# Kernel optimization log

Measured on AMD Instinct MI355X. Metric: run time of the kernel, lower is better.

Reference implementation:

```python
import jax, jax.numpy as jnp
import numpy as np

LSTM = 256
NUM_CELLS = 5
BLOCKS = 6
TEMP = 5.0
TANH_C = 1.1


def setup_inputs() -> dict:
    key = jax.random.key(0)
    ks = jax.random.split(key, 8)
    s = 0.05  # small init so sigmoids/tanh stay in sane range
    return {
        "enc_w": jax.random.normal(ks[0], (5, LSTM), jnp.float32) * s,
        "w_ih": jax.random.normal(ks[1], (4 * LSTM, LSTM), jnp.float32) * s,
        "w_hh": jax.random.normal(ks[2], (4 * LSTM, LSTM), jnp.float32) * s,
        "b_ih": jax.random.normal(ks[3], (4 * LSTM,), jnp.float32) * s,
        "b_hh": jax.random.normal(ks[4], (4 * LSTM,), jnp.float32) * s,
        "w1": jax.random.normal(ks[5], (LSTM, LSTM), jnp.float32) * s,
        "w2": jax.random.normal(ks[6], (LSTM, LSTM), jnp.float32) * s,
        "v": jax.random.normal(ks[7], (LSTM,), jnp.float32) * s,
    }


def _lstm_cell(x, h, c, w_ih, w_hh, b_ih, b_hh):
    # torch.nn.LSTMCell gate order: i, f, g, o
    g = w_ih @ x + b_ih + w_hh @ h + b_hh  # [4*LSTM]
    i, f, gg, o = jnp.split(g, 4)
    i, f, o = jax.nn.sigmoid(i), jax.nn.sigmoid(f), jax.nn.sigmoid(o)
    c2 = f * c + i * jnp.tanh(gg)
    h2 = o * jnp.tanh(c2)
    return h2, c2


def _run_sampler(bkey, enc_w, w_ih, w_hh, b_ih, b_hh, w1, w2, v):
    zeros = jnp.zeros((LSTM,), jnp.float32)
    inputs = enc_w[0]  # encoder(0)
    anchors = []
    anchors_w1 = []
    prev_h = prev_c = zeros
    # first two layers: LSTM always fed zero state (faithful to source)
    for _ in range(2):
        prev_h, prev_c = _lstm_cell(inputs, zeros, zeros, w_ih, w_hh, b_ih, b_hh)
        anchors.append(zeros)
        anchors_w1.append(w1 @ prev_h)
    arc_seq, log_probs, entropies = [], [], []
    step = 0
    for layer_id in range(2, NUM_CELLS + 2):
        for _ in range(2):
            prev_h, prev_c = _lstm_cell(inputs, prev_h, prev_c, w_ih, w_hh, b_ih, b_hh)
            q = jnp.tanh(jnp.stack(anchors_w1[:layer_id]) + w2 @ prev_h)  # [layer_id, LSTM]
            logits = (q @ v) / TEMP  # [layer_id]
            logits = TANH_C * jnp.tanh(logits)
            skey = jax.random.fold_in(bkey, step); step += 1
            index = jax.random.categorical(skey, logits)
            lsm = jax.nn.log_softmax(logits)
            arc_seq.append(index)
            log_probs.append(-lsm[index])  # F.cross_entropy
            entropies.append(jax.lax.stop_gradient(-jnp.sum(lsm * jnp.exp(lsm))))
            inputs = jnp.stack(anchors[:layer_id])[index]
        prev_h, prev_c = _lstm_cell(inputs, prev_h, prev_c, w_ih, w_hh, b_ih, b_hh)
        anchors.append(prev_h)
        anchors_w1.append(w1 @ prev_h)
        inputs = enc_w[0]
    arc = jnp.stack(arc_seq)  # [2*NUM_CELLS] int
    return arc, sum(entropies), sum(log_probs), prev_c, prev_h


def reference(enc_w, w_ih, w_hh, b_ih, b_hh, w1, w2, v):
    key = jax.random.key(42)
    all_arc = []
    all_entropy = jnp.float32(0.0)
    all_log_prob = jnp.float32(0.0)
    c = h = None
    for b in range(BLOCKS):
        arc, ent, lp, c, h = _run_sampler(
            jax.random.fold_in(key, b), enc_w, w_ih, w_hh, b_ih, b_hh, w1, w2, v)
        all_arc.append(arc)
        all_entropy = all_entropy + ent
        all_log_prob = all_log_prob + lp
    return (jnp.stack(all_arc), all_log_prob, all_entropy, c[None, :], h[None, :])
```

## Files before the change

kernel.cpp:

```cpp
#include <hip/hip_runtime.h>
#include <stdint.h>


#define NBLK  6
#define PWG   8
#define TINYF 1.17549435e-38f
#define FXS   67108864.0f
#define READY_MAGIC 0x52454459
#define DONE_MAGIC  0x444f4e45

#define OFF_READY 0u
#define OFF_DONE  192u
#define OFF_PART  224u
#define OFF_HP    320u
#define OFF_ACC   24896u

typedef unsigned long long u64;
struct U2 { uint32_t x, y; };

__device__ __forceinline__ U2 tf2x32(uint32_t k0, uint32_t k1,
                                     uint32_t c0, uint32_t c1) {
  uint32_t ks2 = k0 ^ k1 ^ 0x1BD11BDAu;
  uint32_t x0 = c0 + k0, x1 = c1 + k1;
#define TFR(r) { x0 += x1; x1 = (x1 << (r)) | (x1 >> (32 - (r))); x1 ^= x0; }
  TFR(13) TFR(15) TFR(26) TFR(6)   x0 += k1;  x1 += ks2 + 1u;
  TFR(17) TFR(29) TFR(16) TFR(24)  x0 += ks2; x1 += k0 + 2u;
  TFR(13) TFR(15) TFR(26) TFR(6)   x0 += k0;  x1 += k1 + 3u;
  TFR(17) TFR(29) TFR(16) TFR(24)  x0 += k1;  x1 += ks2 + 4u;
  TFR(13) TFR(15) TFR(26) TFR(6)   x0 += ks2; x1 += k0 + 5u;
#undef TFR
  U2 r; r.x = x0; r.y = x1; return r;
}

__device__ __forceinline__ float sigf(float x) {
  return 1.0f / (1.0f + expf(-x));
}
__device__ __forceinline__ void istore(int* p, int v) {
  __hip_atomic_store(p, v, __ATOMIC_RELAXED, __HIP_MEMORY_SCOPE_AGENT);
}
__device__ __forceinline__ int iload(const int* p) {
  return __hip_atomic_load(p, __ATOMIC_RELAXED, __HIP_MEMORY_SCOPE_AGENT);
}
__device__ __forceinline__ void hstore(u64* p, u64 v) {
  __hip_atomic_store(p, v, __ATOMIC_RELAXED, __HIP_MEMORY_SCOPE_AGENT);
}
__device__ __forceinline__ u64 hload(const u64* p) {
  return __hip_atomic_load(p, __ATOMIC_RELAXED, __HIP_MEMORY_SCOPE_AGENT);
}
__device__ __forceinline__ void fstore(float* p, float v) {
  __hip_atomic_store(p, v, __ATOMIC_RELAXED, __HIP_MEMORY_SCOPE_AGENT);
}
__device__ __forceinline__ float fload(const float* p) {
  return __hip_atomic_load(p, __ATOMIC_RELAXED, __HIP_MEMORY_SCOPE_AGENT);
}

__global__ __launch_bounds__(1024) void ctrl_fused(
    const float* __restrict__ enc_w,
    const float* __restrict__ wih,
    const float* __restrict__ whh,
    const float* __restrict__ b_ih,
    const float* __restrict__ b_hh,
    const float* __restrict__ w1,
    const float* __restrict__ w2,
    const float* __restrict__ vvec,
    unsigned char* __restrict__ ws,
    float* __restrict__ out) {

  const int b = blockIdx.x & 7;
  const int p = blockIdx.x >> 3;
  if (b >= NBLK) return;
  const int tid = threadIdx.x;

  int*   ready = (int*)(ws + OFF_READY);
  int*   done  = (int*)(ws + OFF_DONE);
  float* part  = (float*)(ws + OFF_PART);
  u64*   hp    = (u64*)(ws + OFF_HP);
  int*   acc   = (int*)(ws + OFF_ACC);

  const int rl = tid >> 3, s = tid & 7;
  const int g = rl >> 5, el = rl & 31;
  const int row = g * 256 + p * 32 + el;
  const int k0 = s * 32;
  const int rr = tid & 255, ks = tid >> 2 >> 6;

  __shared__ __align__(16) float hL[256], encL[256], vL[256];
  __shared__ __align__(16) float anchL[4][256];
  __shared__ __align__(16) float partL[1024];
  __shared__ __align__(16) float w2hS[256], aw1S[6][256];
  __shared__ float rowSumL[128], biasS[128], h2S[32];
  __shared__ float logitL[8];
  __shared__ int   selL;

  if (tid < 256) { encL[tid] = enc_w[tid]; vL[tid] = vvec[tid]; }
  if (tid < 128) {
    int gg = tid >> 5, ee = tid & 31, r = gg * 256 + p * 32 + ee;
    biasS[tid] = b_ih[r] + b_hh[r];
  }

  float4 wihr[8], whhr[8];
  #pragma unroll
  for (int c = 0; c < 8; ++c) {
    int cc = (c + s) & 7;
    wihr[c] = *(const float4*)(wih + row * 256 + k0 + cc * 4);
    whhr[c] = *(const float4*)(whh + row * 256 + k0 + cc * 4);
  }
  float w1c[8], w2c[8];
  #pragma unroll
  for (int j = 0; j < 8; ++j) {
    w1c[j] = w1[rr * 256 + p * 32 + ks * 8 + j];
    w2c[j] = w2[rr * 256 + p * 32 + ks * 8 + j];
  }

  if (tid < 32) istore(&acc[1 * (NBLK * 256) + b * 256 + p * 32 + tid], 0);
  __syncthreads();
  if (tid == 0) istore(&ready[b * 8 + p], READY_MAGIC);
  if (tid < 8) {
    while (iload(&ready[b * 8 + tid]) != READY_MAGIC)
      __builtin_amdgcn_s_sleep(1);
  }
  __syncthreads();

  auto dotIH = [&](const float* x) {
    float a = 0.0f;
    #pragma unroll
    for (int c = 0; c < 8; ++c) {
      int cc = (c + s) & 7;
      float4 xv = *(const float4*)(x + k0 + cc * 4);
      float4 w = wihr[c];
      a += w.x * xv.x + w.y * xv.y + w.z * xv.z + w.w * xv.w;
    }
    return a;
  };
  auto dotHH = [&]() {
    float a = 0.0f;
    #pragma unroll
    for (int c = 0; c < 8; ++c) {
      int cc = (c + s) & 7;
      float4 xv = *(const float4*)(hL + k0 + cc * 4);
      float4 w = whhr[c];
      a += w.x * xv.x + w.y * xv.y + w.z * xv.z + w.w * xv.w;
    }
    return a;
  };

  const float encih = dotIH(encL);

  float cv = 0.0f;
  U2 bk = tf2x32(0u, 42u, 0u, (uint32_t)b);
  int k = 1, step = 0;
  float lpAcc = 0.0f, entAcc = 0.0f;

  auto cell = [&](float gacc, int mode, int aid, int cid) {
    partL[tid] = gacc;
    __syncthreads();
    if (tid < 128) {
      float ssum = 0.0f;
      #pragma unroll
      for (int j = 0; j < 8; ++j) ssum += partL[tid * 8 + j];
      rowSumL[tid] = ssum + biasS[tid];
    }
    __syncthreads();
    if (tid < 32) {
      float gi = rowSumL[tid],       gf = rowSumL[32 + tid];
      float gg2 = rowSumL[64 + tid], go = rowSumL[96 + tid];
      float c2 = sigf(gf) * cv + sigf(gi) * tanhf(gg2);
      float h2 = sigf(go) * tanhf(c2);
      cv = c2;
      h2S[tid] = h2;
      if (mode == 2 && b == NBLK - 1) {
        out[62 + p * 32 + tid] = cv;
        out[318 + p * 32 + tid] = h2;
      }
    }
    __syncthreads();
    if (mode == 2) return;

    {
      const float* wc = (mode == 1) ? w1c : w2c;
      float yp = 0.0f;
      #pragma unroll
      for (int j = 0; j < 8; ++j) yp += wc[j] * h2S[ks * 8 + j];
      atomicAdd(&acc[(k % 3) * (NBLK * 256) + b * 256 + rr],
                __float2int_rn(yp * FXS));
      if (tid < 32)
        istore(&acc[((k + 1) % 3) * (NBLK * 256) + b * 256 + p * 32 + tid], 0);
    }
    __syncthreads();
    if (tid < 32) {
      u64 pk = ((u64)(uint32_t)k << 32) | (u64)__float_as_uint(h2S[tid]);
      hstore(&hp[(k & 1) * (NBLK * 256) + b * 256 + p * 32 + tid], pk);
    }
    if (tid < 256) {
      u64 v;
      const u64* src = &hp[(k & 1) * (NBLK * 256) + b * 256 + tid];
      while ((int)(hload(src) >> 32) != k) __builtin_amdgcn_s_sleep(1);
      v = hload(src);
      float hv = __uint_as_float((uint32_t)v);
      hL[tid] = hv;
      if (mode == 1 && cid >= 0) anchL[cid][tid] = hv;
    }
    __syncthreads();
    if (tid < 256) {
      int iv = iload(&acc[(k % 3) * (NBLK * 256) + b * 256 + tid]);
      float f = (float)((double)iv * (1.0 / 67108864.0));
      if (mode == 1) aw1S[aid][tid] = f; else w2hS[tid] = f;
    }
    __syncthreads();
    ++k;
  };

  auto sample = [&](int L) -> int {
    int wv = tid >> 6, lane = tid & 63;
    if (wv < L) {
      float a = 0.0f;
      #pragma unroll
      for (int j = 0; j < 4; ++j) {
        int kk = lane * 4 + j;
        a += tanhf(aw1S[wv][kk] + w2hS[kk]) * vL[kk];
      }
      a += __shfl_down(a, 32);
      a += __shfl_down(a, 16);
      a += __shfl_down(a, 8);
      a += __shfl_down(a, 4);
      a += __shfl_down(a, 2);
      a += __shfl_down(a, 1);
      if (lane == 0) logitL[wv] = a;
    }
    __syncthreads();
    if (tid < 64) {
      float lg = 0.0f, sgum = -1e30f;
      if (tid < L) {
        lg = 1.1f * tanhf(logitL[tid] * 0.2f);
        U2 sk = tf2x32(bk.x, bk.y, 0u, (uint32_t)step);
        U2 r2 = tf2x32(sk.x, sk.y, 0u, (uint32_t)tid);
        uint32_t bits = r2.x ^ r2.y;
        float u = __uint_as_float((bits >> 9) | 0x3f800000u) - 1.0f;
        u = fmaxf(TINYF, u + TINYF);
        sgum = lg - logf(-logf(u));
      }
      int bi = 0;
      float best = __shfl(sgum, 0, 64);
      for (int j = 1; j < L; ++j) {
        float sj = __shfl(sgum, j, 64);
        if (sj > best) { best = sj; bi = j; }
      }
      float mx = __shfl(lg, 0, 64);
      for (int j = 1; j < L; ++j) mx = fmaxf(mx, __shfl(lg, j, 64));
      float se = 0.0f;
      for (int j = 0; j < L; ++j) se += expf(__shfl(lg, j, 64) - mx);
      float lse = logf(se);
      float lgbi = __shfl(lg, bi, 64);
      float es = 0.0f;
      for (int j = 0; j < L; ++j) {
        float l = __shfl(lg, j, 64) - mx - lse;
        es += l * expf(l);
      }
      if (tid == 0) {
        lpAcc += -(lgbi - mx - lse);
        entAcc += -es;
        selL = bi;
        if (p == 0) out[b * 10 + step] = (float)bi;
      }
    }
    __syncthreads();
    step++;
    return selL;
  };

  cell(encih, 1, 0, -1);
  if (tid < 256) aw1S[1][tid] = aw1S[0][tid];
  __syncthreads();

  for (int L = 2; L <= 6; ++L) {
    cell(encih + dotHH(), 0, 0, -1);
    int s1v = sample(L);
    {
      float a = (s1v >= 2) ? dotIH(&anchL[s1v - 2][0]) : 0.0f;
      cell(a + dotHH(), 0, 0, -1);
    }
    int s2v = sample(L);
    {
      float a = (s2v >= 2) ? dotIH(&anchL[s2v - 2][0]) : 0.0f;
      if (L < 6) cell(a + dotHH(), 1, L, L - 2);
      else       cell(a + dotHH(), 2, 0, -1);
    }
  }

  if (p == 0 && tid == 0) {
    fstore(&part[2 * b], lpAcc);
    fstore(&part[2 * b + 1], entAcc);
    __builtin_amdgcn_s_waitcnt(0);
    istore(&done[b], DONE_MAGIC);
    if (b == NBLK - 1) {
      float lp = 0.0f, en = 0.0f;
      for (int j = 0; j < NBLK; ++j) {
        while (iload(&done[j]) != DONE_MAGIC) __builtin_amdgcn_s_sleep(1);
        lp += fload(&part[2 * j]);
        en += fload(&part[2 * j + 1]);
      }
      out[60] = lp;
      out[61] = en;
    }
  }
}

extern "C" void kernel_launch(void* const* d_in, const int* in_sizes, int n_in,
                              void* d_out, int out_size, void* d_ws, size_t ws_size,
                              hipStream_t stream) {
  const float* enc = (const float*)d_in[0];
  const float* wih = (const float*)d_in[1];
  const float* whh = (const float*)d_in[2];
  const float* bih = (const float*)d_in[3];
  const float* bhh = (const float*)d_in[4];
  const float* w1  = (const float*)d_in[5];
  const float* w2  = (const float*)d_in[6];
  const float* v   = (const float*)d_in[7];
  unsigned char* ws = (unsigned char*)d_ws;
  float* out = (float*)d_out;

  ctrl_fused<<<dim3(64), dim3(1024), 0, stream>>>(
      enc, wih, whh, bih, bhh, w1, w2, v, ws, out);
}
```

Measured before the change: 155.7 us.

## Replace atomic fixed-point reductions with tagged per-workgroup partial exchange slots

The cross-workgroup matvec reduction used to be done with integer atomicAdd into triple-buffered accumulators. It now works differently: each workgroup writes its tagged partial sums and h slice into its own slot, and every workgroup polls all eight slots and reduces them locally. This removes the atomic contention, the zeroing of the next buffer, the separate accumulator read phase and the initial ready barrier. Thread-to-row mapping is changed to a strided layout, giving conflict-free shared reductions. The old path is kept as a fallback when the workspace is too small. Tags repeat across launches, so stale slot contents from a previous call could match unless the workspace is cleared.

```diff
diff --git a/kernel.cpp b/kernel.cpp
--- a/kernel.cpp
+++ b/kernel.cpp
@@ -5,18 +5,24 @@
 #define NBLK  6
 #define PWG   8
 #define TINYF 1.17549435e-38f
-#define FXS   67108864.0f
-#define READY_MAGIC 0x52454459
-#define DONE_MAGIC  0x444f4e45
-
-#define OFF_READY 0u
-#define OFF_DONE  192u
-#define OFF_PART  224u
-#define OFF_HP    320u
-#define OFF_ACC   24896u
+#define XTAG  0xC3B00000u
+#define DONE_MAGIC 0x444f4e45
 
 typedef unsigned long long u64;
 struct U2 { uint32_t x, y; };
+
+#define V10_DONE 0u
+#define V10_PART 64u
+#define V10_EX   512u
+#define V10_NEED 221696u
+
+#define S_READY 0u
+#define S_DONE  192u
+#define S_PART  224u
+#define S_HP    320u
+#define S_ACC   24896u
+#define FXS     67108864.0f
+#define READY_MAGIC 0x52454459
 
 __device__ __forceinline__ U2 tf2x32(uint32_t k0, uint32_t k1,
                                      uint32_t c0, uint32_t c1) {
@@ -54,7 +60,7 @@
   return __hip_atomic_load(p, __ATOMIC_RELAXED, __HIP_MEMORY_SCOPE_AGENT);
 }
 
-__global__ __launch_bounds__(1024) void ctrl_fused(
+__global__ __launch_bounds__(1024) void ctrl_v10(
     const float* __restrict__ enc_w,
     const float* __restrict__ wih,
     const float* __restrict__ whh,
@@ -71,21 +77,19 @@
   if (b >= NBLK) return;
   const int tid = threadIdx.x;
 
-  int*   ready = (int*)(ws + OFF_READY);
-  int*   done  = (int*)(ws + OFF_DONE);
-  float* part  = (float*)(ws + OFF_PART);
-  u64*   hp    = (u64*)(ws + OFF_HP);
-  int*   acc   = (int*)(ws + OFF_ACC);
-
-  const int rl = tid >> 3, s = tid & 7;
+  int*   done = (int*)(ws + V10_DONE);
+  float* part = (float*)(ws + V10_PART);
+  u64*   ex   = (u64*)(ws + V10_EX);
+
+  const int rl = tid & 127, s = tid >> 7;
   const int g = rl >> 5, el = rl & 31;
   const int row = g * 256 + p * 32 + el;
   const int k0 = s * 32;
-  const int rr = tid & 255, ks = tid >> 2 >> 6;
-
+  const int rr = tid & 255, ks = tid >> 8;
+
+  __shared__ __align__(16) float gateL[1024];
   __shared__ __align__(16) float hL[256], encL[256], vL[256];
   __shared__ __align__(16) float anchL[4][256];
-  __shared__ __align__(16) float partL[1024];
   __shared__ __align__(16) float w2hS[256], aw1S[6][256];
   __shared__ float rowSumL[128], biasS[128], h2S[32];
   __shared__ float logitL[8];
@@ -93,7 +97,7 @@
 
   if (tid < 256) { encL[tid] = enc_w[tid]; vL[tid] = vvec[tid]; }
   if (tid < 128) {
-    int gg = tid >> 5, ee = tid & 31, r = gg * 256 + p * 32 + ee;
+    int r = (tid >> 5) * 256 + p * 32 + (tid & 31);
     biasS[tid] = b_ih[r] + b_hh[r];
   }
 
@@ -109,14 +113,6 @@
   for (int j = 0; j < 8; ++j) {
     w1c[j] = w1[rr * 256 + p * 32 + ks * 8 + j];
     w2c[j] = w2[rr * 256 + p * 32 + ks * 8 + j];
-  }
-
-  if (tid < 32) istore(&acc[1 * (NBLK * 256) + b * 256 + p * 32 + tid], 0);
-  __syncthreads();
-  if (tid == 0) istore(&ready[b * 8 + p], READY_MAGIC);
-  if (tid < 8) {
-    while (iload(&ready[b * 8 + tid]) != READY_MAGIC)
-      __builtin_amdgcn_s_sleep(1);
   }
   __syncthreads();
 
@@ -151,12 +147,12 @@
   float lpAcc = 0.0f, entAcc = 0.0f;
 
   auto cell = [&](float gacc, int mode, int aid, int cid) {
-    partL[tid] = gacc;
+    gateL[tid] = gacc;
     __syncthreads();
     if (tid < 128) {
       float ssum = 0.0f;
       #pragma unroll
-      for (int j = 0; j < 8; ++j) ssum += partL[tid * 8 + j];
+      for (int j = 0; j < 8; ++j) ssum += gateL[j * 128 + tid];
       rowSumL[tid] = ssum + biasS[tid];
     }
     __syncthreads();
@@ -180,30 +176,46 @@
       float yp = 0.0f;
       #pragma unroll
       for (int j = 0; j < 8; ++j) yp += wc[j] * h2S[ks * 8 + j];
-      atomicAdd(&acc[(k % 3) * (NBLK * 256) + b * 256 + rr],
-                __float2int_rn(yp * FXS));
-      if (tid < 32)
-        istore(&acc[((k + 1) % 3) * (NBLK * 256) + b * 256 + p * 32 + tid], 0);
-    }
-    __syncthreads();
-    if (tid < 32) {
-      u64 pk = ((u64)(uint32_t)k << 32) | (u64)__float_as_uint(h2S[tid]);
-      hstore(&hp[(k & 1) * (NBLK * 256) + b * 256 + p * 32 + tid], pk);
-    }
+      gateL[tid] = yp;
+    }
+    __syncthreads();
+    const uint32_t tagk = XTAG | (uint32_t)k;
+    u64* slot = ex + (((size_t)(k & 1) * NBLK + b) * PWG + p) * 288;
     if (tid < 256) {
-      u64 v;
-      const u64* src = &hp[(k & 1) * (NBLK * 256) + b * 256 + tid];
-      while ((int)(hload(src) >> 32) != k) __builtin_amdgcn_s_sleep(1);
-      v = hload(src);
-      float hv = __uint_as_float((uint32_t)v);
-      hL[tid] = hv;
-      if (mode == 1 && cid >= 0) anchL[cid][tid] = hv;
-    }
-    __syncthreads();
-    if (tid < 256) {
-      int iv = iload(&acc[(k % 3) * (NBLK * 256) + b * 256 + tid]);
-      float f = (float)((double)iv * (1.0 / 67108864.0));
-      if (mode == 1) aw1S[aid][tid] = f; else w2hS[tid] = f;
+      float yo = (gateL[tid] + gateL[256 + tid]) +
+                 (gateL[512 + tid] + gateL[768 + tid]);
+      hstore(slot + tid, ((u64)tagk << 32) | (u64)__float_as_uint(yo));
+    } else if (tid < 288) {
+      hstore(slot + tid,
+             ((u64)tagk << 32) | (u64)__float_as_uint(h2S[tid - 256]));
+    }
+    __syncthreads();
+    {
+      int e = tid & 255, q = tid >> 8;
+      const u64* base = ex + (((size_t)(k & 1) * NBLK + b) * PWG) * 288;
+      const u64* pa = base + (2 * q) * 288 + e;
+      const u64* pb = base + (2 * q + 1) * 288 + e;
+      const u64* ph = base + (tid >> 5) * 288 + 256 + (tid & 31);
+      u64 va = 0, vb = 0, vh = 0;
+      bool da = false, db = false, dh = (tid >= 256);
+      for (;;) {
+        if (!da) { va = hload(pa); da = ((uint32_t)(va >> 32) == tagk); }
+        if (!db) { vb = hload(pb); db = ((uint32_t)(vb >> 32) == tagk); }
+        if (!dh) { vh = hload(ph); dh = ((uint32_t)(vh >> 32) == tagk); }
+        if (da && db && dh) break;
+        __builtin_amdgcn_s_sleep(1);
+      }
+      gateL[tid] = __uint_as_float((uint32_t)va) +
+                   __uint_as_float((uint32_t)vb);
+      float hv = __uint_as_float((uint32_t)vh);
+      __syncthreads();
+      if (tid < 256) {
+        float y = (gateL[tid] + gateL[256 + tid]) +
+                  (gateL[512 + tid] + gateL[768 + tid]);
+        if (mode == 1) aw1S[aid][tid] = y; else w2hS[tid] = y;
+        hL[tid] = hv;
+        if (mode == 1 && cid >= 0) anchL[cid][tid] = hv;
+      }
     }
     __syncthreads();
     ++k;
@@ -215,7 +227,7 @@
       float a = 0.0f;
       #pragma unroll
       for (int j = 0; j < 4; ++j) {
-        int kk = lane * 4 + j;
+        int kk = j * 64 + lane;
         a += tanhf(aw1S[wv][kk] + w2hS[kk]) * vL[kk];
       }
       a += __shfl_down(a, 32);
@@ -286,6 +298,252 @@
     }
   }
 
+  if (p == 0 && tid == 0) {
+    fstore(&part[2 * b], lpAcc);
+    fstore(&part[2 * b + 1], entAcc);
+    __builtin_amdgcn_s_waitcnt(0);
+    istore(&done[b], DONE_MAGIC);
+    if (b == NBLK - 1) {
+      float lp = 0.0f, en = 0.0f;
+      for (int j = 0; j < NBLK; ++j) {
+        while (iload(&done[j]) != DONE_MAGIC) __builtin_amdgcn_s_sleep(1);
+        lp += fload(&part[2 * j]);
+        en += fload(&part[2 * j + 1]);
+      }
+      out[60] = lp;
+      out[61] = en;
+    }
+  }
+}
+
+__global__ __launch_bounds__(1024) void ctrl_small(
+    const float* __restrict__ enc_w,
+    const float* __restrict__ wih,
+    const float* __restrict__ whh,
+    const float* __restrict__ b_ih,
+    const float* __restrict__ b_hh,
+    const float* __restrict__ w1,
+    const float* __restrict__ w2,
+    const float* __restrict__ vvec,
+    unsigned char* __restrict__ ws,
+    float* __restrict__ out) {
+
+  const int b = blockIdx.x & 7;
+  const int p = blockIdx.x >> 3;
+  if (b >= NBLK) return;
+  const int tid = threadIdx.x;
+
+  int*   ready = (int*)(ws + S_READY);
+  int*   done  = (int*)(ws + S_DONE);
+  float* part  = (float*)(ws + S_PART);
+  u64*   hp    = (u64*)(ws + S_HP);
+  int*   acc   = (int*)(ws + S_ACC);
+
+  const int rl = tid >> 3, s = tid & 7;
+  const int g = rl >> 5, el = rl & 31;
+  const int row = g * 256 + p * 32 + el;
+  const int k0 = s * 32;
+  const int rr = tid & 255, ks = tid >> 8;
+
+  __shared__ __align__(16) float hL[256], encL[256], vL[256];
+  __shared__ __align__(16) float anchL[4][256];
+  __shared__ __align__(16) float partL[1024];
+  __shared__ __align__(16) float w2hS[256], aw1S[6][256];
+  __shared__ float rowSumL[128], biasS[128], h2S[32];
+  __shared__ float logitL[8];
+  __shared__ int   selL;
+
+  if (tid < 256) { encL[tid] = enc_w[tid]; vL[tid] = vvec[tid]; }
+  if (tid < 128) {
+    int gg = tid >> 5, ee = tid & 31, r = gg * 256 + p * 32 + ee;
+    biasS[tid] = b_ih[r] + b_hh[r];
+  }
+
+  float4 wihr[8], whhr[8];
+  #pragma unroll
+  for (int c = 0; c < 8; ++c) {
+    int cc = (c + s) & 7;
+    wihr[c] = *(const float4*)(wih + row * 256 + k0 + cc * 4);
+    whhr[c] = *(const float4*)(whh + row * 256 + k0 + cc * 4);
+  }
+  float w1c[8], w2c[8];
+  #pragma unroll
+  for (int j = 0; j < 8; ++j) {
+    w1c[j] = w1[rr * 256 + p * 32 + ks * 8 + j];
+    w2c[j] = w2[rr * 256 + p * 32 + ks * 8 + j];
+  }
+
+  if (tid < 32) istore(&acc[1 * (NBLK * 256) + b * 256 + p * 32 + tid], 0);
+  __syncthreads();
+  if (tid == 0) istore(&ready[b * 8 + p], READY_MAGIC);
+  if (tid < 8) {
+    while (iload(&ready[b * 8 + tid]) != READY_MAGIC)
+      __builtin_amdgcn_s_sleep(1);
+  }
+  __syncthreads();
+
+  auto dotIH = [&](const float* x) {
+    float a = 0.0f;
+    #pragma unroll
+    for (int c = 0; c < 8; ++c) {
+      int cc = (c + s) & 7;
+      float4 xv = *(const float4*)(x + k0 + cc * 4);
+      float4 w = wihr[c];
+      a += w.x * xv.x + w.y * xv.y + w.z * xv.z + w.w * xv.w;
+    }
+    return a;
+  };
+  auto dotHH = [&]() {
+    float a = 0.0f;
+    #pragma unroll
+    for (int c = 0; c < 8; ++c) {
+      int cc = (c + s) & 7;
+      float4 xv = *(const float4*)(hL + k0 + cc * 4);
+      float4 w = whhr[c];
+      a += w.x * xv.x + w.y * xv.y + w.z * xv.z + w.w * xv.w;
+    }
+    return a;
+  };
+
+  const float encih = dotIH(encL);
+  float cv = 0.0f;
+  U2 bk = tf2x32(0u, 42u, 0u, (uint32_t)b);
+  int k = 1, step = 0;
+  float lpAcc = 0.0f, entAcc = 0.0f;
+
+  auto cell = [&](float gacc, int mode, int aid, int cid) {
+    partL[tid] = gacc;
+    __syncthreads();
+    if (tid < 128) {
+      float ssum = 0.0f;
+      #pragma unroll
+      for (int j = 0; j < 8; ++j) ssum += partL[tid * 8 + j];
+      rowSumL[tid] = ssum + biasS[tid];
+    }
+    __syncthreads();
+    if (tid < 32) {
+      float gi = rowSumL[tid],       gf = rowSumL[32 + tid];
+      float gg2 = rowSumL[64 + tid], go = rowSumL[96 + tid];
+      float c2 = sigf(gf) * cv + sigf(gi) * tanhf(gg2);
+      float h2 = sigf(go) * tanhf(c2);
+      cv = c2;
+      h2S[tid] = h2;
+      if (mode == 2 && b == NBLK - 1) {
+        out[62 + p * 32 + tid] = cv;
+        out[318 + p * 32 + tid] = h2;
+      }
+    }
+    __syncthreads();
+    if (mode == 2) return;
+    {
+      const float* wc = (mode == 1) ? w1c : w2c;
+      float yp = 0.0f;
+      #pragma unroll
+      for (int j = 0; j < 8; ++j) yp += wc[j] * h2S[ks * 8 + j];
+      atomicAdd(&acc[(k % 3) * (NBLK * 256) + b * 256 + rr],
+                __float2int_rn(yp * FXS));
+      if (tid < 32)
+        istore(&acc[((k + 1) % 3) * (NBLK * 256) + b * 256 + p * 32 + tid], 0);
+    }
+    __syncthreads();
+    if (tid < 32) {
+      u64 pk = ((u64)(uint32_t)k << 32) | (u64)__float_as_uint(h2S[tid]);
+      hstore(&hp[(k & 1) * (NBLK * 256) + b * 256 + p * 32 + tid], pk);
+    }
+    if (tid < 256) {
+      u64 v;
+      const u64* src = &hp[(k & 1) * (NBLK * 256) + b * 256 + tid];
+      while ((int)(hload(src) >> 32) != k) __builtin_amdgcn_s_sleep(1);
+      v = hload(src);
+      float hv = __uint_as_float((uint32_t)v);
+      hL[tid] = hv;
+      if (mode == 1 && cid >= 0) anchL[cid][tid] = hv;
+    }
+    __syncthreads();
+    if (tid < 256) {
+      int iv = iload(&acc[(k % 3) * (NBLK * 256) + b * 256 + tid]);
+      float f = (float)((double)iv * (1.0 / 67108864.0));
+      if (mode == 1) aw1S[aid][tid] = f; else w2hS[tid] = f;
+    }
+    __syncthreads();
+    ++k;
+  };
+
+  auto sample = [&](int L) -> int {
+    int wv = tid >> 6, lane = tid & 63;
+    if (wv < L) {
+      float a = 0.0f;
+      #pragma unroll
+      for (int j = 0; j < 4; ++j) {
+        int kk = lane * 4 + j;
+        a += tanhf(aw1S[wv][kk] + w2hS[kk]) * vL[kk];
+      }
+      a += __shfl_down(a, 32);
+      a += __shfl_down(a, 16);
+      a += __shfl_down(a, 8);
+      a += __shfl_down(a, 4);
+      a += __shfl_down(a, 2);
+      a += __shfl_down(a, 1);
+      if (lane == 0) logitL[wv] = a;
+    }
+    __syncthreads();
+    if (tid < 64) {
+      float lg = 0.0f, sgum = -1e30f;
+      if (tid < L) {
+        lg = 1.1f * tanhf(logitL[tid] * 0.2f);
+        U2 sk = tf2x32(bk.x, bk.y, 0u, (uint32_t)step);
+        U2 r2 = tf2x32(sk.x, sk.y, 0u, (uint32_t)tid);
+        uint32_t bits = r2.x ^ r2.y;
+        float u = __uint_as_float((bits >> 9) | 0x3f800000u) - 1.0f;
+        u = fmaxf(TINYF, u + TINYF);
+        sgum = lg - logf(-logf(u));
+      }
+      int bi = 0;
+      float best = __shfl(sgum, 0, 64);
+      for (int j = 1; j < L; ++j) {
+        float sj = __shfl(sgum, j, 64);
+        if (sj > best) { best = sj; bi = j; }
+      }
+      float mx = __shfl(lg, 0, 64);
+      for (int j = 1; j < L; ++j) mx = fmaxf(mx, __shfl(lg, j, 64));
+      float se = 0.0f;
+      for (int j = 0; j < L; ++j) se += expf(__shfl(lg, j, 64) - mx);
+      float lse = logf(se);
+      float lgbi = __shfl(lg, bi, 64);
+      float es = 0.0f;
+      for (int j = 0; j < L; ++j) {
+        float l = __shfl(lg, j, 64) - mx - lse;
+        es += l * expf(l);
+      }
+      if (tid == 0) {
+        lpAcc += -(lgbi - mx - lse);
+        entAcc += -es;
+        selL = bi;
+        if (p == 0) out[b * 10 + step] = (float)bi;
+      }
+    }
+    __syncthreads();
+    step++;
+    return selL;
+  };
+
+  cell(encih, 1, 0, -1);
+  if (tid < 256) aw1S[1][tid] = aw1S[0][tid];
+  __syncthreads();
+  for (int L = 2; L <= 6; ++L) {
+    cell(encih + dotHH(), 0, 0, -1);
+    int s1v = sample(L);
+    {
+      float a = (s1v >= 2) ? dotIH(&anchL[s1v - 2][0]) : 0.0f;
+      cell(a + dotHH(), 0, 0, -1);
+    }
+    int s2v = sample(L);
+    {
+      float a = (s2v >= 2) ? dotIH(&anchL[s2v - 2][0]) : 0.0f;
+      if (L < 6) cell(a + dotHH(), 1, L, L - 2);
+      else       cell(a + dotHH(), 2, 0, -1);
+    }
+  }
   if (p == 0 && tid == 0) {
     fstore(&part[2 * b], lpAcc);
     fstore(&part[2 * b + 1], entAcc);
@@ -318,6 +576,11 @@
   unsigned char* ws = (unsigned char*)d_ws;
   float* out = (float*)d_out;
 
-  ctrl_fused<<<dim3(64), dim3(1024), 0, stream>>>(
-      enc, wih, whh, bih, bhh, w1, w2, v, ws, out);
-}
+  if (ws_size >= V10_NEED) {
+    ctrl_v10<<<dim3(64), dim3(1024), 0, stream>>>(
+        enc, wih, whh, bih, bhh, w1, w2, v, ws, out);
+  } else {
+    ctrl_small<<<dim3(64), dim3(1024), 0, stream>>>(
+        enc, wih, whh, bih, bhh, w1, w2, v, ws, out);
+  }
+}
```

Result: no change. 158.3 us (+1.7%).
